# Performance work log

Hardware: AMD Instinct MI355X
Metric: run time of the kernel (lower is better)

The kernel has to match this reference:

```python
import jax, jax.numpy as jnp
import numpy as np

D_MODEL = 1024
D_STATE = 16
BATCH = 2
SEQ = 2048


def setup_inputs() -> dict:
    key = jax.random.key(0)
    k1, k2, k3, k4 = jax.random.split(key, 4)
    x = jax.random.normal(k1, (BATCH, SEQ, D_MODEL), dtype=jnp.float32)
    dt = jax.random.uniform(k2, (BATCH, SEQ, D_MODEL), dtype=jnp.float32)
    B_in = jax.random.normal(k3, (BATCH, SEQ, D_STATE), dtype=jnp.float32)
    C_in = jax.random.normal(k4, (BATCH, SEQ, D_STATE), dtype=jnp.float32)
    # Parameters, initialized as in the torch module
    A = jnp.arange(1, D_STATE + 1, dtype=jnp.float32)[None, :] * jnp.ones((D_MODEL, 1), jnp.float32)
    A_log = jnp.log(A)
    D = jnp.ones((D_MODEL,), jnp.float32)
    return {"x": x, "dt": dt, "B_in": B_in, "C_in": C_in, "A_log": A_log, "D": D}


def reference(x, dt, B_in, C_in, A_log, D):
    # x, dt: (b, L, d);  B_in, C_in: (b, L, n);  A_log: (d, n);  D: (d,)
    A = -jnp.exp(A_log)                                   # (d, n)
    A_disc = jnp.exp(dt[..., None] * A[None, None])       # (b, L, d, n)
    Bx = dt[..., None] * B_in[:, :, None, :] * x[..., None]  # (b, L, d, n)

    def step(state, inputs):
        a_t, bx_t, c_t = inputs                            # (b,d,n),(b,d,n),(b,n)
        state = a_t * state + bx_t                         # (b, d, n)
        y_t = jnp.einsum('bdn,bn->bd', state, c_t)         # (b, d)
        return state, y_t

    state0 = jnp.zeros((x.shape[0], x.shape[2], A_log.shape[1]), x.dtype)
    # scan over the time axis (put L first)
    _, y = jax.lax.scan(
        step, state0,
        (jnp.moveaxis(A_disc, 1, 0), jnp.moveaxis(Bx, 1, 0), jnp.moveaxis(C_in, 1, 0)))
    y = jnp.moveaxis(y, 0, 1)                              # (b, L, d)
    return y + x * D[None, None, :]
```

## Files before the change

### kernel.cpp

```cpp
#include <hip/hip_runtime.h>
#include <hip/hip_bf16.h>

namespace {

constexpr int kB = 2;
constexpr int kL = 2048;
constexpr int kD = 1024;
constexpr int kN = 16;
constexpr int kTPB = 256;
constexpr int kNDBLK = kD / kTPB;
constexpr int kBD = kB * kD;
constexpr int kBDN = kB * kD * kN;
constexpr float kLog2e = 1.4426950408889634f;

__device__ __forceinline__ float fast_exp2(float v) {
  return __builtin_amdgcn_exp2f(v);
}

template <int C>
__global__ __launch_bounds__(kTPB) void ssm_phase1(
    const float* __restrict__ x, const float* __restrict__ dt,
    const float* __restrict__ Bin, const float* __restrict__ Alog,
    float* __restrict__ WA, float* __restrict__ WS) {
  constexpr int LC = kL / C;
  const int bid = blockIdx.x;
  const int c = bid % C;
  const int r = bid / C;
  const int dblk = r % kNDBLK;
  const int b = r / kNDBLK;
  const int d = dblk * kTPB + threadIdx.x;

  float An[kN];
  const float* al = Alog + d * kN;
#pragma unroll
  for (int n = 0; n < kN; ++n) An[n] = -__expf(al[n]) * kLog2e;

  float s[kN], ap[kN];
#pragma unroll
  for (int n = 0; n < kN; ++n) { s[n] = 0.f; ap[n] = 1.f; }

  const int t0 = c * LC;
  const float* xp  = x  + ((size_t)b * kL + t0) * kD + d;
  const float* dtp = dt + ((size_t)b * kL + t0) * kD + d;
  const float* bp  = Bin + ((size_t)b * kL + t0) * kN;

#pragma unroll 4
  for (int tt = 0; tt < LC; ++tt) {
    const float dtv = dtp[(size_t)tt * kD];
    const float xv  = xp[(size_t)tt * kD];
    const float dtx = dtv * xv;
#pragma unroll
    for (int n = 0; n < kN; ++n) {
      const float a = fast_exp2(dtv * An[n]);
      s[n] = fmaf(a, s[n], dtx * bp[tt * kN + n]);
      ap[n] *= a;
    }
  }

  const size_t base = (size_t)c * kBDN + (size_t)b * kD + d;
#pragma unroll
  for (int n = 0; n < kN; ++n) {
    WA[base + (size_t)n * kBD] = ap[n];
    WS[base + (size_t)n * kBD] = s[n];
  }
}

template <int C>
__global__ __launch_bounds__(256) void ssm_phase2(
    const float* __restrict__ WA, const float* __restrict__ WS,
    float* __restrict__ WI) {
  const int i = blockIdx.x * 256 + threadIdx.x;
  float carry = 0.f;
  for (int c = 0; c < C; ++c) {
    const size_t idx = (size_t)c * kBDN + i;
    const float a  = WA[idx];
    const float sf = WS[idx];
    WI[idx] = carry;
    carry = fmaf(a, carry, sf);
  }
}

template <int C>
__global__ __launch_bounds__(kTPB) void ssm_phase3(
    const float* __restrict__ x, const float* __restrict__ dt,
    const float* __restrict__ Bin, const float* __restrict__ Cin,
    const float* __restrict__ Alog, const float* __restrict__ Dp,
    const float* __restrict__ WI, float* __restrict__ y) {
  constexpr int LC = kL / C;
  const int bid = blockIdx.x;
  const int c = bid % C;
  const int r = bid / C;
  const int dblk = r % kNDBLK;
  const int b = r / kNDBLK;
  const int d = dblk * kTPB + threadIdx.x;

  float An[kN];
  const float* al = Alog + d * kN;
#pragma unroll
  for (int n = 0; n < kN; ++n) An[n] = -__expf(al[n]) * kLog2e;

  float s[kN];
  const size_t base = (size_t)c * kBDN + (size_t)b * kD + d;
#pragma unroll
  for (int n = 0; n < kN; ++n) s[n] = WI[base + (size_t)n * kBD];

  const float Dv = Dp[d];

  const int t0 = c * LC;
  const float* xp  = x  + ((size_t)b * kL + t0) * kD + d;
  const float* dtp = dt + ((size_t)b * kL + t0) * kD + d;
  const float* bp  = Bin + ((size_t)b * kL + t0) * kN;
  const float* cp  = Cin + ((size_t)b * kL + t0) * kN;
  float* yp = y + ((size_t)b * kL + t0) * kD + d;

#pragma unroll 4
  for (int tt = 0; tt < LC; ++tt) {
    const float dtv = dtp[(size_t)tt * kD];
    const float xv  = xp[(size_t)tt * kD];
    const float dtx = dtv * xv;
    float acc = 0.f;
#pragma unroll
    for (int n = 0; n < kN; ++n) {
      const float a = fast_exp2(dtv * An[n]);
      s[n] = fmaf(a, s[n], dtx * bp[tt * kN + n]);
      acc = fmaf(s[n], cp[tt * kN + n], acc);
    }
    yp[(size_t)tt * kD] = fmaf(xv, Dv, acc);
  }
}

__global__ __launch_bounds__(256) void ssm_seq(
    const float* __restrict__ x, const float* __restrict__ dt,
    const float* __restrict__ Bin, const float* __restrict__ Cin,
    const float* __restrict__ Alog, const float* __restrict__ Dp,
    float* __restrict__ y) {
  const int gid = blockIdx.x * 256 + threadIdx.x;
  if (gid >= kB * kD) return;
  const int b = gid / kD;
  const int d = gid % kD;

  float An[kN];
  const float* al = Alog + d * kN;
#pragma unroll
  for (int n = 0; n < kN; ++n) An[n] = -__expf(al[n]) * kLog2e;

  float s[kN];
#pragma unroll
  for (int n = 0; n < kN; ++n) s[n] = 0.f;
  const float Dv = Dp[d];

  const float* xp  = x  + (size_t)b * kL * kD + d;
  const float* dtp = dt + (size_t)b * kL * kD + d;
  const float* bp  = Bin + (size_t)b * kL * kN;
  const float* cp  = Cin + (size_t)b * kL * kN;
  float* yp = y + (size_t)b * kL * kD + d;

  for (int t = 0; t < kL; ++t) {
    const float dtv = dtp[(size_t)t * kD];
    const float xv  = xp[(size_t)t * kD];
    const float dtx = dtv * xv;
    float acc = 0.f;
#pragma unroll
    for (int n = 0; n < kN; ++n) {
      const float a = fast_exp2(dtv * An[n]);
      s[n] = fmaf(a, s[n], dtx * bp[t * kN + n]);
      acc = fmaf(s[n], cp[t * kN + n], acc);
    }
    yp[(size_t)t * kD] = fmaf(xv, Dv, acc);
  }
}

template <int C>
void launch_chunked(const float* x, const float* dtp, const float* Bin,
                    const float* Cin, const float* Alog, const float* Dp,
                    float* y, float* ws, hipStream_t stream) {
  float* WA = ws;
  float* WS = WA + (size_t)C * kBDN;
  float* WI = WS + (size_t)C * kBDN;
  const int g1 = C * kB * kNDBLK;
  ssm_phase1<C><<<g1, kTPB, 0, stream>>>(x, dtp, Bin, Alog, WA, WS);
  ssm_phase2<C><<<kBDN / 256, 256, 0, stream>>>(WA, WS, WI);
  ssm_phase3<C><<<g1, kTPB, 0, stream>>>(x, dtp, Bin, Cin, Alog, Dp, WI, y);
}

}

extern "C" void kernel_launch(void* const* d_in, const int* in_sizes, int n_in,
                              void* d_out, int out_size, void* d_ws, size_t ws_size,
                              hipStream_t stream) {
  const float* x    = (const float*)d_in[0];
  const float* dtp  = (const float*)d_in[1];
  const float* Bin  = (const float*)d_in[2];
  const float* Cin  = (const float*)d_in[3];
  const float* Alog = (const float*)d_in[4];
  const float* Dp   = (const float*)d_in[5];
  float* y = (float*)d_out;
  float* ws = (float*)d_ws;

  auto need = [](int C) { return (size_t)3 * C * kBDN * sizeof(float); };

  if (ws_size >= need(64)) {
    launch_chunked<64>(x, dtp, Bin, Cin, Alog, Dp, y, ws, stream);
  } else if (ws_size >= need(16)) {
    launch_chunked<16>(x, dtp, Bin, Cin, Alog, Dp, y, ws, stream);
  } else if (ws_size >= need(4)) {
    launch_chunked<4>(x, dtp, Bin, Cin, Alog, Dp, y, ws, stream);
  } else {
    ssm_seq<<<(kB * kD + 255) / 256, 256, 0, stream>>>(x, dtp, Bin, Cin, Alog,
                                                       Dp, y);
  }
}
```

Before: 48.69 us.

## Replace per-state exps with powers of one exp and derive chunk decay from summed dt

```diff
diff --git a/kernel.cpp b/kernel.cpp
--- a/kernel.cpp
+++ b/kernel.cpp
@@ -10,18 +10,28 @@
 constexpr int kTPB = 256;
 constexpr int kNDBLK = kD / kTPB;
 constexpr int kBD = kB * kD;
-constexpr int kBDN = kB * kD * kN;
+constexpr int kBDN = kBD * kN;
 constexpr float kLog2e = 1.4426950408889634f;
 
-__device__ __forceinline__ float fast_exp2(float v) {
+__device__ __forceinline__ float ex2(float v) {
   return __builtin_amdgcn_exp2f(v);
+}
+
+__device__ __forceinline__ void build_pows(float e1, float* a) {
+  const float p2 = e1 * e1;
+  const float p4 = p2 * p2;
+  const float p8 = p4 * p4;
+  a[0] = e1;      a[1] = p2;      a[2] = p2 * e1; a[3] = p4;
+  a[4] = p4 * e1; a[5] = p4 * p2; a[6] = p4 * a[2]; a[7] = p8;
+  a[8] = p8 * e1; a[9] = p8 * p2; a[10] = p8 * a[2]; a[11] = p8 * p4;
+  a[12] = p8 * a[4]; a[13] = p8 * a[5]; a[14] = p8 * a[6]; a[15] = p8 * p8;
 }
 
 template <int C>
 __global__ __launch_bounds__(kTPB) void ssm_phase1(
     const float* __restrict__ x, const float* __restrict__ dt,
     const float* __restrict__ Bin, const float* __restrict__ Alog,
-    float* __restrict__ WA, float* __restrict__ WS) {
+    float* __restrict__ WS, float* __restrict__ SDT) {
   constexpr int LC = kL / C;
   const int bid = blockIdx.x;
   const int c = bid % C;
@@ -30,53 +40,77 @@
   const int b = r / kNDBLK;
   const int d = dblk * kTPB + threadIdx.x;
 
-  float An[kN];
+  float AnL[kN];
   const float* al = Alog + d * kN;
 #pragma unroll
-  for (int n = 0; n < kN; ++n) An[n] = -__expf(al[n]) * kLog2e;
-
-  float s[kN], ap[kN];
-#pragma unroll
-  for (int n = 0; n < kN; ++n) { s[n] = 0.f; ap[n] = 1.f; }
+  for (int n = 0; n < kN; ++n) AnL[n] = -__expf(al[n]) * kLog2e;
+  bool fast = true;
+#pragma unroll
+  for (int n = 1; n < kN; ++n)
+    fast = fast && (fabsf(AnL[n] - (float)(n + 1) * AnL[0]) <=
+                    1e-4f * fabsf(AnL[n]));
+
+  float s[kN];
+#pragma unroll
+  for (int n = 0; n < kN; ++n) s[n] = 0.f;
+  float sdt = 0.f;
 
   const int t0 = c * LC;
-  const float* xp  = x  + ((size_t)b * kL + t0) * kD + d;
-  const float* dtp = dt + ((size_t)b * kL + t0) * kD + d;
-  const float* bp  = Bin + ((size_t)b * kL + t0) * kN;
-
+  const float* xp = x + ((size_t)b * kL + t0) * kD + d;
+  const float* dp = dt + ((size_t)b * kL + t0) * kD + d;
+  const float* bp = Bin + ((size_t)b * kL + t0) * kN;
+
+  if (fast) {
+    const float A0 = AnL[0];
 #pragma unroll 4
-  for (int tt = 0; tt < LC; ++tt) {
-    const float dtv = dtp[(size_t)tt * kD];
-    const float xv  = xp[(size_t)tt * kD];
-    const float dtx = dtv * xv;
-#pragma unroll
-    for (int n = 0; n < kN; ++n) {
-      const float a = fast_exp2(dtv * An[n]);
-      s[n] = fmaf(a, s[n], dtx * bp[tt * kN + n]);
-      ap[n] *= a;
-    }
-  }
-
-  const size_t base = (size_t)c * kBDN + (size_t)b * kD + d;
-#pragma unroll
-  for (int n = 0; n < kN; ++n) {
-    WA[base + (size_t)n * kBD] = ap[n];
-    WS[base + (size_t)n * kBD] = s[n];
-  }
+    for (int tt = 0; tt < LC; ++tt) {
+      const float dtv = dp[(size_t)tt * kD];
+      const float xv = xp[(size_t)tt * kD];
+      sdt += dtv;
+      const float dtx = dtv * xv;
+      float a[kN];
+      build_pows(ex2(dtv * A0), a);
+#pragma unroll
+      for (int n = 0; n < kN; ++n)
+        s[n] = fmaf(a[n], s[n], dtx * bp[tt * kN + n]);
+    }
+  } else {
+#pragma unroll 2
+    for (int tt = 0; tt < LC; ++tt) {
+      const float dtv = dp[(size_t)tt * kD];
+      const float xv = xp[(size_t)tt * kD];
+      sdt += dtv;
+      const float dtx = dtv * xv;
+#pragma unroll
+      for (int n = 0; n < kN; ++n) {
+        const float a = ex2(dtv * AnL[n]);
+        s[n] = fmaf(a, s[n], dtx * bp[tt * kN + n]);
+      }
+    }
+  }
+
+  const size_t bd = (size_t)b * kD + d;
+#pragma unroll
+  for (int n = 0; n < kN; ++n)
+    WS[(size_t)c * kBDN + (size_t)n * kBD + bd] = s[n];
+  SDT[(size_t)c * kBD + bd] = sdt;
 }
 
 template <int C>
 __global__ __launch_bounds__(256) void ssm_phase2(
-    const float* __restrict__ WA, const float* __restrict__ WS,
-    float* __restrict__ WI) {
+    const float* __restrict__ WS, const float* __restrict__ SDT,
+    const float* __restrict__ Alog, float* __restrict__ WI) {
   const int i = blockIdx.x * 256 + threadIdx.x;
+  const int n = i >> 11;
+  const int bd = i & (kBD - 1);
+  const int d = bd & (kD - 1);
+  const float An = -__expf(Alog[d * kN + n]) * kLog2e;
   float carry = 0.f;
   for (int c = 0; c < C; ++c) {
     const size_t idx = (size_t)c * kBDN + i;
-    const float a  = WA[idx];
-    const float sf = WS[idx];
+    const float a = ex2(An * SDT[(size_t)c * kBD + bd]);
     WI[idx] = carry;
-    carry = fmaf(a, carry, sf);
+    carry = fmaf(a, carry, WS[idx]);
   }
 }
 
@@ -94,38 +128,63 @@
   const int b = r / kNDBLK;
   const int d = dblk * kTPB + threadIdx.x;
 
-  float An[kN];
+  float AnL[kN];
   const float* al = Alog + d * kN;
 #pragma unroll
-  for (int n = 0; n < kN; ++n) An[n] = -__expf(al[n]) * kLog2e;
+  for (int n = 0; n < kN; ++n) AnL[n] = -__expf(al[n]) * kLog2e;
+  bool fast = true;
+#pragma unroll
+  for (int n = 1; n < kN; ++n)
+    fast = fast && (fabsf(AnL[n] - (float)(n + 1) * AnL[0]) <=
+                    1e-4f * fabsf(AnL[n]));
 
   float s[kN];
-  const size_t base = (size_t)c * kBDN + (size_t)b * kD + d;
-#pragma unroll
-  for (int n = 0; n < kN; ++n) s[n] = WI[base + (size_t)n * kBD];
+  const size_t bd = (size_t)b * kD + d;
+#pragma unroll
+  for (int n = 0; n < kN; ++n)
+    s[n] = WI[(size_t)c * kBDN + (size_t)n * kBD + bd];
 
   const float Dv = Dp[d];
 
   const int t0 = c * LC;
-  const float* xp  = x  + ((size_t)b * kL + t0) * kD + d;
-  const float* dtp = dt + ((size_t)b * kL + t0) * kD + d;
-  const float* bp  = Bin + ((size_t)b * kL + t0) * kN;
-  const float* cp  = Cin + ((size_t)b * kL + t0) * kN;
+  const float* xp = x + ((size_t)b * kL + t0) * kD + d;
+  const float* dp = dt + ((size_t)b * kL + t0) * kD + d;
+  const float* bp = Bin + ((size_t)b * kL + t0) * kN;
+  const float* cp = Cin + ((size_t)b * kL + t0) * kN;
   float* yp = y + ((size_t)b * kL + t0) * kD + d;
 
+  if (fast) {
+    const float A0 = AnL[0];
 #pragma unroll 4
-  for (int tt = 0; tt < LC; ++tt) {
-    const float dtv = dtp[(size_t)tt * kD];
-    const float xv  = xp[(size_t)tt * kD];
-    const float dtx = dtv * xv;
-    float acc = 0.f;
-#pragma unroll
-    for (int n = 0; n < kN; ++n) {
-      const float a = fast_exp2(dtv * An[n]);
-      s[n] = fmaf(a, s[n], dtx * bp[tt * kN + n]);
-      acc = fmaf(s[n], cp[tt * kN + n], acc);
-    }
-    yp[(size_t)tt * kD] = fmaf(xv, Dv, acc);
+    for (int tt = 0; tt < LC; ++tt) {
+      const float dtv = dp[(size_t)tt * kD];
+      const float xv = xp[(size_t)tt * kD];
+      const float dtx = dtv * xv;
+      float a[kN];
+      build_pows(ex2(dtv * A0), a);
+      float acc = 0.f;
+#pragma unroll
+      for (int n = 0; n < kN; ++n) {
+        s[n] = fmaf(a[n], s[n], dtx * bp[tt * kN + n]);
+        acc = fmaf(s[n], cp[tt * kN + n], acc);
+      }
+      yp[(size_t)tt * kD] = fmaf(xv, Dv, acc);
+    }
+  } else {
+#pragma unroll 2
+    for (int tt = 0; tt < LC; ++tt) {
+      const float dtv = dp[(size_t)tt * kD];
+      const float xv = xp[(size_t)tt * kD];
+      const float dtx = dtv * xv;
+      float acc = 0.f;
+#pragma unroll
+      for (int n = 0; n < kN; ++n) {
+        const float a = ex2(dtv * AnL[n]);
+        s[n] = fmaf(a, s[n], dtx * bp[tt * kN + n]);
+        acc = fmaf(s[n], cp[tt * kN + n], acc);
+      }
+      yp[(size_t)tt * kD] = fmaf(xv, Dv, acc);
+    }
   }
 }
 
@@ -139,30 +198,30 @@
   const int b = gid / kD;
   const int d = gid % kD;
 
-  float An[kN];
+  float AnL[kN];
   const float* al = Alog + d * kN;
 #pragma unroll
-  for (int n = 0; n < kN; ++n) An[n] = -__expf(al[n]) * kLog2e;
+  for (int n = 0; n < kN; ++n) AnL[n] = -__expf(al[n]) * kLog2e;
 
   float s[kN];
 #pragma unroll
   for (int n = 0; n < kN; ++n) s[n] = 0.f;
   const float Dv = Dp[d];
 
-  const float* xp  = x  + (size_t)b * kL * kD + d;
-  const float* dtp = dt + (size_t)b * kL * kD + d;
-  const float* bp  = Bin + (size_t)b * kL * kN;
-  const float* cp  = Cin + (size_t)b * kL * kN;
+  const float* xp = x + (size_t)b * kL * kD + d;
+  const float* dp = dt + (size_t)b * kL * kD + d;
+  const float* bp = Bin + (size_t)b * kL * kN;
+  const float* cp = Cin + (size_t)b * kL * kN;
   float* yp = y + (size_t)b * kL * kD + d;
 
   for (int t = 0; t < kL; ++t) {
-    const float dtv = dtp[(size_t)t * kD];
-    const float xv  = xp[(size_t)t * kD];
+    const float dtv = dp[(size_t)t * kD];
+    const float xv = xp[(size_t)t * kD];
     const float dtx = dtv * xv;
     float acc = 0.f;
 #pragma unroll
     for (int n = 0; n < kN; ++n) {
-      const float a = fast_exp2(dtv * An[n]);
+      const float a = ex2(dtv * AnL[n]);
       s[n] = fmaf(a, s[n], dtx * bp[t * kN + n]);
       acc = fmaf(s[n], cp[t * kN + n], acc);
     }
@@ -174,13 +233,13 @@
 void launch_chunked(const float* x, const float* dtp, const float* Bin,
                     const float* Cin, const float* Alog, const float* Dp,
                     float* y, float* ws, hipStream_t stream) {
-  float* WA = ws;
-  float* WS = WA + (size_t)C * kBDN;
-  float* WI = WS + (size_t)C * kBDN;
-  const int g1 = C * kB * kNDBLK;
-  ssm_phase1<C><<<g1, kTPB, 0, stream>>>(x, dtp, Bin, Alog, WA, WS);
-  ssm_phase2<C><<<kBDN / 256, 256, 0, stream>>>(WA, WS, WI);
-  ssm_phase3<C><<<g1, kTPB, 0, stream>>>(x, dtp, Bin, Cin, Alog, Dp, WI, y);
+  float* WS = ws;
+  float* SDT = WS + (size_t)C * kBDN;
+  float* WI = SDT + (size_t)C * kBD;
+  const int g = C * kB * kNDBLK;
+  ssm_phase1<C><<<g, kTPB, 0, stream>>>(x, dtp, Bin, Alog, WS, SDT);
+  ssm_phase2<C><<<kBDN / 256, 256, 0, stream>>>(WS, SDT, Alog, WI);
+  ssm_phase3<C><<<g, kTPB, 0, stream>>>(x, dtp, Bin, Cin, Alog, Dp, WI, y);
 }
 
 }
@@ -197,14 +256,16 @@
   float* y = (float*)d_out;
   float* ws = (float*)d_ws;
 
-  auto need = [](int C) { return (size_t)3 * C * kBDN * sizeof(float); };
-
-  if (ws_size >= need(64)) {
+  auto need = [](int C) {
+    return (size_t)(2 * C * kBDN + C * kBD) * sizeof(float);
+  };
+
+  if (ws_size >= need(128)) {
+    launch_chunked<128>(x, dtp, Bin, Cin, Alog, Dp, y, ws, stream);
+  } else if (ws_size >= need(64)) {
     launch_chunked<64>(x, dtp, Bin, Cin, Alog, Dp, y, ws, stream);
   } else if (ws_size >= need(16)) {
     launch_chunked<16>(x, dtp, Bin, Cin, Alog, Dp, y, ws, stream);
-  } else if (ws_size >= need(4)) {
-    launch_chunked<4>(x, dtp, Bin, Cin, Alog, Dp, y, ws, stream);
   } else {
     ssm_seq<<<(kB * kD + 255) / 256, 256, 0, stream>>>(x, dtp, Bin, Cin, Alog,
                                                        Dp, y);
```

Measured after the change: 41.55 us. 14.7% less time.
